# Kernel tuning notes

Measured on AMD Instinct MI355X. Metric: run time of the kernel, lower is better.

Reference implementation:

```python
import jax, jax.numpy as jnp
import numpy as np

IMG_H, IMG_W = 1024, 1024
STRIDES = (8, 16, 32, 64, 128)
NUM_CLASSES = 80
CONF_THR = 0.05
IOU_THR = 0.5
MAX_PER_CLASS = 100
MAX_DET = 100
K_CAND = 256  # candidates kept per class before greedy NMS (pre-sort cap)


def build_grids():
    gy, gx, gs = [], [], []
    for s in STRIDES:
        H, W = IMG_H // s, IMG_W // s
        h = jnp.arange(H, dtype=jnp.float32)
        w = jnp.arange(W, dtype=jnp.float32)
        gy_, gx_ = jnp.meshgrid(h, w)  # 'xy' indexing -> shape [W, H], matches tf.meshgrid
        gy.append(gy_.reshape(-1))
        gx.append(gx_.reshape(-1))
        gs.append(jnp.full((W * H,), float(s), dtype=jnp.float32))
    return jnp.concatenate(gy), jnp.concatenate(gx), jnp.concatenate(gs)


def pairwise_iou(b):
    # b: [K,4] as (y1, x1, y2, x2)
    y1, x1, y2, x2 = b[:, 0], b[:, 1], b[:, 2], b[:, 3]
    area = (y2 - y1) * (x2 - x1)
    ih = jnp.maximum(jnp.minimum(y2[:, None], y2[None, :]) - jnp.maximum(y1[:, None], y1[None, :]), 0.0)
    iw = jnp.maximum(jnp.minimum(x2[:, None], x2[None, :]) - jnp.maximum(x1[:, None], x1[None, :]), 0.0)
    inter = ih * iw
    union = area[:, None] + area[None, :] - inter
    return inter / jnp.maximum(union, 1e-8)


def nms_one_class(boxes, scores):
    # boxes [N,4], scores [N] -> (sel_boxes [MAX_PER_CLASS,4], sel_scores [MAX_PER_CLASS])
    top_s, idx = jax.lax.top_k(scores, K_CAND)
    cand = boxes[idx]                       # [K,4]
    valid = top_s > CONF_THR
    iou = jax.lax.stop_gradient(pairwise_iou(cand))  # suppression mask is non-differentiable
    rng = jnp.arange(K_CAND)

    def body(i, keep):
        sup = (iou[i] > IOU_THR) & (rng > i) & keep[i]
        return keep & ~sup

    keep = jax.lax.fori_loop(0, K_CAND, body, valid)
    kept = jnp.where(keep, top_s, 0.0)
    sel_s, sel_i = jax.lax.top_k(kept, MAX_PER_CLASS)
    return cand[sel_i], sel_s


def combined_nms(boxes, scores):
    # per image: boxes [N,4] shared across classes, scores [N,C]
    cls_boxes, cls_scores = jax.vmap(nms_one_class, in_axes=(None, 1))(boxes, scores)
    C = scores.shape[1]
    cls_labels = jnp.broadcast_to(jnp.arange(C, dtype=jnp.float32)[:, None], cls_scores.shape)
    flat_s = cls_scores.reshape(-1)
    flat_b = cls_boxes.reshape(-1, 4)
    flat_l = cls_labels.reshape(-1)
    fin_s, fin_i = jax.lax.top_k(flat_s, MAX_DET)
    fin_b = flat_b[fin_i] * (fin_s > 0.0)[:, None].astype(flat_b.dtype)  # zero pad boxes like TF
    fin_l = flat_l[fin_i]
    return fin_b, fin_l, fin_s


def decode(pred_regs, pred_ctrs, pred_clfs):
    gy, gx, gs = build_grids()
    gy, gx, gs = gy[:, None], gx[:, None], gs[:, None]     # [N,1]
    score = pred_clfs * pred_ctrs                           # [B,N,C]
    x1 = gx - pred_regs[..., 0:1]
    x2 = gx + pred_regs[..., 1:2]
    y1 = gy - pred_regs[..., 2:3]
    y2 = gy + pred_regs[..., 3:4]
    bbox = jnp.concatenate([y1, x1, y2, x2], axis=-1) * gs  # [B,N,4] in image coords
    return jax.vmap(combined_nms)(bbox, score)


def setup_inputs() -> dict:
    key = jax.random.key(0)
    k1, k2, k3 = jax.random.split(key, 3)
    N = sum((IMG_H // s) * (IMG_W // s) for s in STRIDES)  # 21824
    B = 16
    return {
        "pred_regs": jax.random.uniform(k1, (B, N, 4), jnp.float32),
        "pred_ctrs": jax.random.uniform(k2, (B, N, 1), jnp.float32),
        "pred_clfs": jax.random.uniform(k3, (B, N, NUM_CLASSES), jnp.float32),
    }


def reference(pred_regs, pred_ctrs, pred_clfs):
    # returns (final_bboxes [B,100,4], final_labels [B,100] float, final_scores [B,100])
    return decode(pred_regs, pred_ctrs, pred_clfs)
```

## Files before the change

### kernel.cpp

```cpp
#include <hip/hip_runtime.h>
#include <stdint.h>

#pragma clang fp contract(off)

namespace {
constexpr int kN = 21824;
constexpr int kB = 16;
constexpr int kC = 80;
constexpr int kK = 256;
constexpr int kMaxPC = 100;
constexpr int kMaxDet = 100;
constexpr int kBins1 = 2048;
constexpr int kCap = 1536;
constexpr int kSortN = 512;
constexpr int kRows = kB * kC;
constexpr int kTiles = kN / 64;
constexpr int kTPB = 6;
constexpr int kGScan = (kTiles + kTPB - 1) / kTPB;
constexpr int kLCap = 48;
constexpr float kThr = 0.72f;
constexpr int kTasks = 1152;
}

__device__ __forceinline__ uint64_t make_key(float s, int n) {
  return ((uint64_t)__float_as_uint(s) << 16) | (uint32_t)(0xFFFF - n);
}

__device__ uint32_t block_scan_incl(uint32_t val) {
  __shared__ uint32_t wsum[4];
  int lane = threadIdx.x & 63;
  int wave = threadIdx.x >> 6;
  for (int d = 1; d < 64; d <<= 1) {
    uint32_t t = __shfl_up(val, (unsigned)d, 64);
    if (lane >= d) val += t;
  }
  if (lane == 63) wsum[wave] = val;
  __syncthreads();
  uint32_t off = 0;
  for (int w = 0; w < wave; ++w) off += wsum[w];
  __syncthreads();
  return val + off;
}

struct RegSrc {
  uint64_t k[6];
  int cnt;
  template <class F> __device__ void each(F f) const {
    #pragma unroll
    for (int j = 0; j < 6; ++j)
      if (j < cnt) f(k[j]);
  }
  template <class F> __device__ void each2(F f) const {
    #pragma unroll
    for (int j = 0; j < 6; ++j) f(k[j], j < cnt);
  }
};
struct ColSrc {
  const float* cl;
  const float* ct;
  template <class F> __device__ void each(F f) const {
    for (int n = threadIdx.x; n < kN; n += 256)
      f(make_key(cl[(size_t)n * kC] * ct[n], n));
  }
  template <class F> __device__ void each2(F f) const {
    constexpr int kNr = (kN + 255) & ~255;
    for (int n = threadIdx.x; n < kNr; n += 256) {
      bool v = n < kN;
      float s = v ? cl[(size_t)n * kC] * ct[n] : 0.0f;
      f(make_key(s, n), v);
    }
  }
};
struct ArrSrc {
  const float* s;
  int count;
  template <class F> __device__ void each(F f) const {
    for (int i = threadIdx.x; i < count; i += 256) f(make_key(s[i], i));
  }
  template <class F> __device__ void each2(F f) const {
    int cr = (count + 255) & ~255;
    for (int i = threadIdx.x; i < cr; i += 256) {
      bool v = i < count;
      float sv = v ? s[i] : 0.0f;
      f(make_key(sv, i), v);
    }
  }
};

template <class Src, bool FAST>
__device__ int refine_gather(const Src& src, int K, int cap,
                             uint32_t* hist, uint64_t* cbuf) {
  __shared__ int sel_bin;
  __shared__ uint32_t sel_hd, sel_above, qcnt;
  int tid = threadIdx.x;

  for (int i = tid; i < kBins1; i += 256) hist[i] = 0;
  __syncthreads();
  src.each([&](uint64_t k) {
    uint32_t bin = FAST ? (uint32_t)((k >> 28) & 0x7FF) : (uint32_t)(k >> 37);
    atomicAdd(&hist[bin], 1u);
  });
  __syncthreads();
  uint32_t krem = (uint32_t)K;
  {
    uint32_t bl[8], v = 0;
    int base = kBins1 - 1 - 8 * tid;
    for (int j = 0; j < 8; ++j) { bl[j] = hist[base - j]; v += bl[j]; }
    uint32_t S = block_scan_incl(v);
    if (S >= krem && (S - v) < krem) {
      uint32_t cum = S - v;
      for (int j = 0; j < 8; ++j) {
        cum += bl[j];
        if (cum >= krem) { sel_bin = base - j; sel_hd = bl[j]; sel_above = cum - bl[j]; break; }
      }
    }
    __syncthreads();
  }
  uint64_t prefix = FAST ? (uint64_t)(0x3F000u | (uint32_t)sel_bin)
                         : (uint64_t)sel_bin;
  int shift = FAST ? 28 : 37;
  krem = (uint32_t)K - sel_above;
  uint32_t Sge = ((uint32_t)K - krem) + sel_hd;
  __syncthreads();

  while (Sge > (uint32_t)cap) {
    int w = (shift > 8) ? 8 : shift;
    int ns = shift - w, bins = 1 << w, hs = shift;
    for (int i = tid; i < bins; i += 256) hist[i] = 0;
    __syncthreads();
    uint64_t pfx = prefix;
    src.each([&](uint64_t k) {
      if ((k >> hs) == pfx)
        atomicAdd(&hist[(uint32_t)(k >> ns) & (bins - 1)], 1u);
    });
    __syncthreads();
    uint32_t v = (tid < bins) ? hist[bins - 1 - tid] : 0;
    uint32_t S = block_scan_incl(v);
    if (v && S >= krem && (S - v) < krem) {
      sel_bin = bins - 1 - tid; sel_hd = v; sel_above = S - v;
    }
    __syncthreads();
    prefix = (prefix << w) | (uint32_t)sel_bin;
    krem -= sel_above;
    Sge = ((uint32_t)K - krem) + sel_hd;
    shift = ns;
    __syncthreads();
  }

  uint64_t L = prefix << shift;
  if (tid == 0) qcnt = 0;
  __syncthreads();
  {
    int lane = tid & 63;
    uint64_t lmask = (1ull << lane) - 1ull;
    src.each2([&](uint64_t k, bool valid) {
      bool q = valid && (k >= L);
      unsigned long long m = __ballot(q);
      uint32_t base = 0;
      if (lane == 0 && m) base = atomicAdd(&qcnt, (uint32_t)__popcll(m));
      base = __shfl(base, 0, 64);
      if (q) {
        uint32_t p = base + (uint32_t)__popcll(m & lmask);
        if (p < (uint32_t)cap) cbuf[p] = k;
      }
    });
  }
  __syncthreads();
  int Scnt = (int)qcnt;
  return Scnt > cap ? cap : Scnt;
}

__device__ __forceinline__ void bitonic512_desc(uint64_t* sortb) {
  int tid = threadIdx.x;
  uint64_t e0 = sortb[2 * tid], e1 = sortb[2 * tid + 1];
  #pragma unroll
  for (int k2 = 2; k2 <= kSortN; k2 <<= 1) {
    #pragma unroll
    for (int j = k2 >> 1; j >= 2; j >>= 1) {
      bool up = ((tid & (k2 >> 1)) == 0);
      uint64_t p0, p1;
      bool low;
      if (j >= 128) {
        __syncthreads();
        sortb[2 * tid] = e0; sortb[2 * tid + 1] = e1;
        __syncthreads();
        int pi = (2 * tid) ^ j;
        p0 = sortb[pi]; p1 = sortb[pi + 1];
        low = ((tid & (j >> 1)) == 0);
      } else {
        int d = j >> 1;
        p0 = (uint64_t)__shfl_xor((unsigned long long)e0, d, 64);
        p1 = (uint64_t)__shfl_xor((unsigned long long)e1, d, 64);
        low = ((tid & d) == 0);
      }
      bool keepMax = (up == low);
      e0 = (keepMax == (e0 > p0)) ? e0 : p0;
      e1 = (keepMax == (e1 > p1)) ? e1 : p1;
    }
    {
      bool up = ((tid & (k2 >> 1)) == 0);
      bool sw = up ? (e0 < e1) : (e0 > e1);
      uint64_t t0 = sw ? e1 : e0, t1 = sw ? e0 : e1;
      e0 = t0; e1 = t1;
    }
  }
  __syncthreads();
  sortb[2 * tid] = e0; sortb[2 * tid + 1] = e1;
  __syncthreads();
}

__global__ __launch_bounds__(256) void score_scan_kernel(
    const float* __restrict__ clfs, const float* __restrict__ ctrs,
    uint32_t* __restrict__ gcnt, uint64_t* __restrict__ glist) {
  int b = blockIdx.y;
  int t0 = blockIdx.x * kTPB;
  int t1 = t0 + kTPB; if (t1 > kTiles) t1 = kTiles;
  int nbase = t0 * 64;
  int nanch = (t1 - t0) * 64;

  __shared__ uint64_t lbuf[kC][kLCap + 1];
  __shared__ uint32_t lcnt[kC];
  __shared__ uint32_t gbase[kC];
  __shared__ float ct[kTPB * 64];
  int tid = threadIdx.x;
  for (int i = tid; i < kC; i += 256) lcnt[i] = 0;
  for (int i = tid; i < nanch; i += 256) ct[i] = ctrs[(size_t)b * kN + nbase + i];
  __syncthreads();

  const float4* src = (const float4*)(clfs + ((size_t)b * kN + nbase) * kC);
  int n4 = nanch * (kC / 4);
  float4 v = (tid < n4) ? src[tid] : float4{0, 0, 0, 0};
  for (int e = tid; e < n4; e += 256) {
    int en = e + 256;
    float4 vn = (en < n4) ? src[en] : float4{0, 0, 0, 0};
    int a = e / 20;
    int c0 = (e % 20) * 4;
    float cv = ct[a];
    int n = nbase + a;
    float sv[4] = {v.x * cv, v.y * cv, v.z * cv, v.w * cv};
    #pragma unroll
    for (int j = 0; j < 4; ++j) {
      if (sv[j] > kThr) {
        int c = c0 + j;
        uint32_t p = atomicAdd(&lcnt[c], 1u);
        if (p < kLCap) lbuf[c][p] = make_key(sv[j], n);
      }
    }
    v = vn;
  }
  __syncthreads();

  if (tid < kC) {
    uint32_t m = lcnt[tid];
    int row = b * kC + tid;
    if (m > kLCap) {
      atomicAdd(&gcnt[row], (uint32_t)(kCap + 1));
      gbase[tid] = 0xFFFFFFFFu;
    } else {
      gbase[tid] = m ? atomicAdd(&gcnt[row], m) : 0u;
    }
  }
  __syncthreads();

  int lane = tid & 63, wave = tid >> 6;
  for (int c = wave * 20; c < wave * 20 + 20; ++c) {
    uint32_t m = lcnt[c];
    uint32_t base = gbase[c];
    if (base == 0xFFFFFFFFu || m == 0) continue;
    if (m > kLCap) m = kLCap;
    int row = b * kC + c;
    for (uint32_t i = lane; i < m; i += 64) {
      uint32_t p = base + i;
      if (p < kCap) glist[(size_t)row * kCap + p] = lbuf[c][i];
    }
  }
}

__global__ __launch_bounds__(256) void nms_class_kernel(
    const uint32_t* __restrict__ gcnt, const uint64_t* __restrict__ glist,
    const float* __restrict__ clfs, const float* __restrict__ ctrs,
    const float* __restrict__ regs,
    float* __restrict__ cls_boxes, float* __restrict__ cls_scores) {
  int row = blockIdx.x;
  int b = row / kC, c = row % kC;
  int tid = threadIdx.x;
  int lane = tid & 63, wave = tid >> 6;

  __shared__ union alignas(16) {
    uint32_t hist[kBins1];
    uint64_t sortb[kSortN];
    uint32_t supm[kK][8];
  } hu;
  __shared__ float4 boxf4[kK];
  __shared__ float barea[kK];
  __shared__ uint32_t rnz[8];
  __shared__ uint64_t kinit[4];
  __shared__ uint64_t kfin[4];

  uint32_t cnt = gcnt[row];
  int Scnt;
  if (cnt >= (uint32_t)kK && cnt <= (uint32_t)kCap) {
    RegSrc rs; rs.cnt = 0;
    const uint64_t* gl = glist + (size_t)row * kCap;
    #pragma unroll
    for (int j = 0; j < 6; ++j) {
      int i = tid + j * 256;
      if (i < (int)cnt) { rs.k[j] = gl[i]; rs.cnt = j + 1; }
    }
    Scnt = refine_gather<RegSrc, true>(rs, kK, kSortN, hu.hist, hu.sortb);
  } else {
    ColSrc cs{clfs + (size_t)b * kN * kC + c, ctrs + (size_t)b * kN};
    Scnt = refine_gather<ColSrc, false>(cs, kK, kSortN, hu.hist, hu.sortb);
  }

  for (int i = Scnt + tid; i < kSortN; i += 256) hu.sortb[i] = 0;
  __syncthreads();
  bitonic512_desc(hu.sortb);
  uint64_t myk = hu.sortb[tid];
  __syncthreads();

  int n = 0xFFFF - (int)(myk & 0xFFFF);
  float sc_v = __uint_as_float((uint32_t)(myk >> 16));
  int off, hl;
  float sf;
  if (n < 16384)      { off = 0;     hl = 7; sf = 8.f;   }
  else if (n < 20480) { off = 16384; hl = 6; sf = 16.f;  }
  else if (n < 21504) { off = 20480; hl = 5; sf = 32.f;  }
  else if (n < 21760) { off = 21504; hl = 4; sf = 64.f;  }
  else                { off = 21760; hl = 3; sf = 128.f; }
  int kk = n - off;
  float gx = (float)(kk >> hl);
  float gy = (float)(kk & ((1 << hl) - 1));
  const float4 r = ((const float4*)regs)[(size_t)b * kN + n];
  float4 mybox;
  mybox.x = (gy - r.z) * sf;
  mybox.y = (gx - r.x) * sf;
  mybox.z = (gy + r.w) * sf;
  mybox.w = (gx + r.y) * sf;
  float my_a = (mybox.z - mybox.x) * (mybox.w - mybox.y);
  boxf4[tid] = mybox;
  barea[tid] = my_a;
  unsigned long long vm = __ballot(sc_v > 0.05f);
  if (lane == 0) kinit[wave] = vm;
  {
    uint64_t* sp = (uint64_t*)&hu.supm[0][0];
    #pragma unroll
    for (int q = 0; q < 4; ++q) sp[tid + q * 256] = 0;
    if (tid < 8) rnz[tid] = 0;
  }
  __syncthreads();

  for (int t = tid; t < kTasks; t += 256) {
    int w = (t >= 32) + (t >= 96) + (t >= 192) + (t >= 320) +
            (t >= 480) + (t >= 672) + (t >= 896);
    int rr = t - 16 * w * (w + 1);
    float4 A = boxf4[rr];
    float aA = barea[rr];
    const float4* bp = boxf4 + (w << 5);
    const float* ap = barea + (w << 5);
    uint32_t cur = 0;
    #pragma unroll
    for (int s = 0; s < 32; ++s) {
      const float4 Bx = bp[s];
      float aB = ap[s];
      float yy1 = fmaxf(A.x, Bx.x);
      float yy2 = fminf(A.z, Bx.z);
      float xx1 = fmaxf(A.y, Bx.y);
      float xx2 = fminf(A.w, Bx.w);
      float ih = fmaxf(yy2 - yy1, 0.0f);
      float iw = fmaxf(xx2 - xx1, 0.0f);
      float inter = ih * iw;
      float un = (aB + aA) - inter;
      float unc = fmaxf(un, 1e-8f);
      cur |= (inter + inter > unc) ? (1u << s) : 0u;
    }
    uint32_t mask = (w == (rr >> 5)) ? (0xFFFFFFFEu << (rr & 31)) : 0xFFFFFFFFu;
    cur &= mask;
    hu.supm[rr][w] = cur;
    if (cur) atomicOr(&rnz[rr >> 5], 1u << (rr & 31));
  }
  __syncthreads();

  if (wave == 0) {
    uint64_t kw0 = kinit[0], kw1 = kinit[1], kw2 = kinit[2], kw3 = kinit[3];
    uint64_t wn0 = rnz[0] | ((uint64_t)rnz[1] << 32);
    uint64_t wn1 = rnz[2] | ((uint64_t)rnz[3] << 32);
    uint64_t wn2 = rnz[4] | ((uint64_t)rnz[5] << 32);
    uint64_t wn3 = rnz[6] | ((uint64_t)rnz[7] << 32);
    #define NMS_SECTION(W, KW, WN)                                          \
      _Pragma("unroll")                                                     \
      for (int ch = 0; ch < 16; ++ch) {                                     \
        if ((WN >> (ch * 4)) & 0xFull) {                                    \
          const ulonglong2* s0 = (const ulonglong2*)hu.supm[(W << 6) + ch * 4 + 0]; \
          const ulonglong2* s1 = (const ulonglong2*)hu.supm[(W << 6) + ch * 4 + 1]; \
          const ulonglong2* s2 = (const ulonglong2*)hu.supm[(W << 6) + ch * 4 + 2]; \
          const ulonglong2* s3 = (const ulonglong2*)hu.supm[(W << 6) + ch * 4 + 3]; \
          ulonglong2 aL = s0[0], aH = s0[1];                                \
          ulonglong2 bL = s1[0], bH = s1[1];                                \
          ulonglong2 cL = s2[0], cH = s2[1];                                \
          ulonglong2 dL = s3[0], dH = s3[1];                                \
          if ((KW >> (ch * 4 + 0)) & 1ull) { kw0 &= ~aL.x; kw1 &= ~aL.y; kw2 &= ~aH.x; kw3 &= ~aH.y; } \
          if ((KW >> (ch * 4 + 1)) & 1ull) { kw0 &= ~bL.x; kw1 &= ~bL.y; kw2 &= ~bH.x; kw3 &= ~bH.y; } \
          if ((KW >> (ch * 4 + 2)) & 1ull) { kw0 &= ~cL.x; kw1 &= ~cL.y; kw2 &= ~cH.x; kw3 &= ~cH.y; } \
          if ((KW >> (ch * 4 + 3)) & 1ull) { kw0 &= ~dL.x; kw1 &= ~dL.y; kw2 &= ~dH.x; kw3 &= ~dH.y; } \
        }                                                                   \
      }
    NMS_SECTION(0, kw0, wn0)
    NMS_SECTION(1, kw1, wn1)
    NMS_SECTION(2, kw2, wn2)
    NMS_SECTION(3, kw3, wn3)
    #undef NMS_SECTION
    if (lane == 0) { kfin[0] = kw0; kfin[1] = kw1; kfin[2] = kw2; kfin[3] = kw3; }
  }
  __syncthreads();

  uint64_t kw0 = kfin[0], kw1 = kfin[1], kw2 = kfin[2], kw3 = kfin[3];
  uint64_t ww = (wave == 0) ? kw0 : (wave == 1) ? kw1 : (wave == 2) ? kw2 : kw3;
  bool keptf = (ww >> lane) & 1ull;
  int kept_total = (int)(__popcll(kw0) + __popcll(kw1) +
                         __popcll(kw2) + __popcll(kw3));
  int kept_before = (int)__popcll(ww & ((1ull << lane) - 1ull));
  if (wave > 0) kept_before += (int)__popcll(kw0);
  if (wave > 1) kept_before += (int)__popcll(kw1);
  if (wave > 2) kept_before += (int)__popcll(kw2);

  int rank2 = keptf ? kept_before : (kept_total + tid - kept_before);
  if (rank2 < kMaxPC) {
    float ks = keptf ? sc_v : 0.0f;
    size_t obase = ((size_t)row) * kMaxPC + rank2;
    cls_scores[obase] = ks;
    float* ob = cls_boxes + obase * 4;
    ob[0] = mybox.x; ob[1] = mybox.y; ob[2] = mybox.z; ob[3] = mybox.w;
  }
}

__global__ __launch_bounds__(256) void final_topk_kernel(
    const float* __restrict__ cls_scores, const float* __restrict__ cls_boxes,
    float* __restrict__ out) {
  int b = blockIdx.x;
  int tid = threadIdx.x;
  const int M = kC * kMaxPC;
  __shared__ union alignas(16) {
    uint32_t hist[kBins1];
    uint64_t sortb[kSortN];
  } hu;

  ArrSrc as{cls_scores + (size_t)b * M, M};
  int Scnt = refine_gather<ArrSrc, false>(as, kMaxDet, kSortN, hu.hist, hu.sortb);

  for (int i = Scnt + tid; i < kSortN; i += 256) hu.sortb[i] = 0;
  __syncthreads();
  bitonic512_desc(hu.sortb);

  if (tid < kMaxDet) {
    uint64_t myk = hu.sortb[tid];
    float sv = __uint_as_float((uint32_t)(myk >> 16));
    int f = 0xFFFF - (int)(myk & 0xFFFF);
    int cls = f / 100;
    const float* bp = cls_boxes + ((size_t)b * M + f) * 4;
    float m = (sv > 0.0f) ? 1.0f : 0.0f;
    float* ob = out + ((size_t)b * kMaxDet + tid) * 4;
    ob[0] = bp[0] * m; ob[1] = bp[1] * m; ob[2] = bp[2] * m; ob[3] = bp[3] * m;
    out[(size_t)kB * kMaxDet * 4 + (size_t)b * kMaxDet + tid] = (float)cls;
    out[(size_t)kB * kMaxDet * 5 + (size_t)b * kMaxDet + tid] = sv;
  }
}

extern "C" void kernel_launch(void* const* d_in, const int* in_sizes, int n_in,
                              void* d_out, int out_size, void* d_ws, size_t ws_size,
                              hipStream_t stream) {
  (void)in_sizes; (void)n_in; (void)out_size;
  const float* regs = (const float*)d_in[0];
  const float* ctrs = (const float*)d_in[1];
  const float* clfs = (const float*)d_in[2];
  float* out = (float*)d_out;

  const size_t glB  = (size_t)kRows * kCap * sizeof(uint64_t);
  const size_t cbB  = (size_t)kRows * kMaxPC * 4 * sizeof(float);
  const size_t csB  = (size_t)kRows * kMaxPC * sizeof(float);
  const size_t cntB = 8192;
  if (ws_size < glB + cbB + csB + cntB) return;

  char* p = (char*)d_ws;
  uint64_t* glist   = (uint64_t*)p; p += glB;
  float* cls_boxes  = (float*)p;    p += cbB;
  float* cls_scores = (float*)p;    p += csB;
  uint32_t* gcnt    = (uint32_t*)p;

  hipMemsetAsync(gcnt, 0, (size_t)kRows * sizeof(uint32_t), stream);
  score_scan_kernel<<<dim3(kGScan, kB), 256, 0, stream>>>(clfs, ctrs, gcnt, glist);
  nms_class_kernel<<<kRows, 256, 0, stream>>>(gcnt, glist, clfs, ctrs, regs,
                                              cls_boxes, cls_scores);
  final_topk_kernel<<<kB, 256, 0, stream>>>(cls_scores, cls_boxes, out);
}
```

Before: 242.9 us.

## Fuse final top-k into NMS kernel via last-block counter and prefetch box regs

Removes the separate final_topk launch: each class block increments a per-image counter after a threadfence, and the last block for that image runs the final top-k inline. The candidate keys now carry their gather slot index, so box regressions can be loaded and decoded before the bitonic sort and looked up by slot afterwards, overlapping global latency with the sort. The score scan also replaces the per-element divide and modulo with incremental index tracking. In exchange the tail work becomes serialized in one block per image, and there is an extra shared buffer and barrier.

Result: slower. 352.1 us (+45.0%).

```diff
diff --git a/kernel.cpp b/kernel.cpp
--- a/kernel.cpp
+++ b/kernel.cpp
@@ -161,7 +161,7 @@
       base = __shfl(base, 0, 64);
       if (q) {
         uint32_t p = base + (uint32_t)__popcll(m & lmask);
-        if (p < (uint32_t)cap) cbuf[p] = k;
+        if (p < (uint32_t)cap) cbuf[p] = (k << 16) | p;
       }
     });
   }
@@ -209,6 +209,25 @@
   __syncthreads();
 }
 
+__device__ __forceinline__ float4 decode_box(const float4& r, int n) {
+  int off, hl;
+  float sf;
+  if (n < 16384)      { off = 0;     hl = 7; sf = 8.f;   }
+  else if (n < 20480) { off = 16384; hl = 6; sf = 16.f;  }
+  else if (n < 21504) { off = 20480; hl = 5; sf = 32.f;  }
+  else if (n < 21760) { off = 21504; hl = 4; sf = 64.f;  }
+  else                { off = 21760; hl = 3; sf = 128.f; }
+  int kk = n - off;
+  float gx = (float)(kk >> hl);
+  float gy = (float)(kk & ((1 << hl) - 1));
+  float4 bx;
+  bx.x = (gy - r.z) * sf;
+  bx.y = (gx - r.x) * sf;
+  bx.z = (gy + r.w) * sf;
+  bx.w = (gx + r.y) * sf;
+  return bx;
+}
+
 __global__ __launch_bounds__(256) void score_scan_kernel(
     const float* __restrict__ clfs, const float* __restrict__ ctrs,
     uint32_t* __restrict__ gcnt, uint64_t* __restrict__ glist) {
@@ -230,11 +249,12 @@
   const float4* src = (const float4*)(clfs + ((size_t)b * kN + nbase) * kC);
   int n4 = nanch * (kC / 4);
   float4 v = (tid < n4) ? src[tid] : float4{0, 0, 0, 0};
+  int a = tid / 20;
+  int rem = tid - a * 20;
   for (int e = tid; e < n4; e += 256) {
     int en = e + 256;
     float4 vn = (en < n4) ? src[en] : float4{0, 0, 0, 0};
-    int a = e / 20;
-    int c0 = (e % 20) * 4;
+    int c0 = rem * 4;
     float cv = ct[a];
     int n = nbase + a;
     float sv[4] = {v.x * cv, v.y * cv, v.z * cv, v.w * cv};
@@ -247,6 +267,8 @@
       }
     }
     v = vn;
+    a += 12; rem += 16;
+    if (rem >= 20) { rem -= 20; ++a; }
   }
   __syncthreads();
 
@@ -276,11 +298,36 @@
   }
 }
 
+__device__ void final_topk_block(int b, const float* cls_scores,
+                                 const float* cls_boxes, float* out,
+                                 uint32_t* hist, uint64_t* sbuf) {
+  int tid = threadIdx.x;
+  const int M = kC * kMaxPC;
+  ArrSrc as{cls_scores + (size_t)b * M, M};
+  int Scnt = refine_gather<ArrSrc, false>(as, kMaxDet, kSortN, hist, sbuf);
+  for (int i = Scnt + tid; i < kSortN; i += 256) sbuf[i] = 0;
+  __syncthreads();
+  bitonic512_desc(sbuf);
+  if (tid < kMaxDet) {
+    uint64_t myk = sbuf[tid] >> 16;
+    float sv = __uint_as_float((uint32_t)(myk >> 16));
+    int f = 0xFFFF - (int)(myk & 0xFFFF);
+    int cls = f / 100;
+    const float* bp = cls_boxes + ((size_t)b * M + f) * 4;
+    float m = (sv > 0.0f) ? 1.0f : 0.0f;
+    float* ob = out + ((size_t)b * kMaxDet + tid) * 4;
+    ob[0] = bp[0] * m; ob[1] = bp[1] * m; ob[2] = bp[2] * m; ob[3] = bp[3] * m;
+    out[(size_t)kB * kMaxDet * 4 + (size_t)b * kMaxDet + tid] = (float)cls;
+    out[(size_t)kB * kMaxDet * 5 + (size_t)b * kMaxDet + tid] = sv;
+  }
+}
+
 __global__ __launch_bounds__(256) void nms_class_kernel(
-    const uint32_t* __restrict__ gcnt, const uint64_t* __restrict__ glist,
+    uint32_t* gcnt, const uint64_t* __restrict__ glist,
     const float* __restrict__ clfs, const float* __restrict__ ctrs,
     const float* __restrict__ regs,
-    float* __restrict__ cls_boxes, float* __restrict__ cls_scores) {
+    float* __restrict__ cls_boxes, float* __restrict__ cls_scores,
+    float* __restrict__ out) {
   int row = blockIdx.x;
   int b = row / kC, c = row % kC;
   int tid = threadIdx.x;
@@ -288,14 +335,16 @@
 
   __shared__ union alignas(16) {
     uint32_t hist[kBins1];
-    uint64_t sortb[kSortN];
     uint32_t supm[kK][8];
+    float4 boxq[kSortN];
   } hu;
+  __shared__ uint64_t sbuf[kSortN];
   __shared__ float4 boxf4[kK];
   __shared__ float barea[kK];
   __shared__ uint32_t rnz[8];
   __shared__ uint64_t kinit[4];
   __shared__ uint64_t kfin[4];
+  __shared__ uint32_t bflag;
 
   uint32_t cnt = gcnt[row];
   int Scnt;
@@ -307,41 +356,42 @@
       int i = tid + j * 256;
       if (i < (int)cnt) { rs.k[j] = gl[i]; rs.cnt = j + 1; }
     }
-    Scnt = refine_gather<RegSrc, true>(rs, kK, kSortN, hu.hist, hu.sortb);
+    Scnt = refine_gather<RegSrc, true>(rs, kK, kSortN, hu.hist, sbuf);
   } else {
     ColSrc cs{clfs + (size_t)b * kN * kC + c, ctrs + (size_t)b * kN};
-    Scnt = refine_gather<ColSrc, false>(cs, kK, kSortN, hu.hist, hu.sortb);
-  }
-
-  for (int i = Scnt + tid; i < kSortN; i += 256) hu.sortb[i] = 0;
-  __syncthreads();
-  bitonic512_desc(hu.sortb);
-  uint64_t myk = hu.sortb[tid];
-  __syncthreads();
-
-  int n = 0xFFFF - (int)(myk & 0xFFFF);
+    Scnt = refine_gather<ColSrc, false>(cs, kK, kSortN, hu.hist, sbuf);
+  }
+
+  for (int i = Scnt + tid; i < kSortN; i += 256) sbuf[i] = 0;
+  __syncthreads();
+
+  uint64_t E0 = sbuf[2 * tid], E1 = sbuf[2 * tid + 1];
+  int p0 = (int)(E0 & 0xFFFF), p1 = (int)(E1 & 0xFFFF);
+  int a0 = 0xFFFF - (int)((E0 >> 16) & 0xFFFF);
+  int a1 = 0xFFFF - (int)((E1 >> 16) & 0xFFFF);
+  int a0v = (E0 != 0) ? a0 : 0;
+  int a1v = (E1 != 0) ? a1 : 0;
+  const float4* rp = (const float4*)regs + (size_t)b * kN;
+  float4 r0 = rp[a0v];
+  float4 r1 = rp[a1v];
+
+  bitonic512_desc(sbuf);
+
+  if (E0 != 0) hu.boxq[p0] = decode_box(r0, a0v);
+  if (E1 != 0) hu.boxq[p1] = decode_box(r1, a1v);
+  __syncthreads();
+
+  uint64_t ku = sbuf[tid];
+  uint32_t qidx = (uint32_t)(ku & 0xFFFF);
+  uint64_t myk = ku >> 16;
   float sc_v = __uint_as_float((uint32_t)(myk >> 16));
-  int off, hl;
-  float sf;
-  if (n < 16384)      { off = 0;     hl = 7; sf = 8.f;   }
-  else if (n < 20480) { off = 16384; hl = 6; sf = 16.f;  }
-  else if (n < 21504) { off = 20480; hl = 5; sf = 32.f;  }
-  else if (n < 21760) { off = 21504; hl = 4; sf = 64.f;  }
-  else                { off = 21760; hl = 3; sf = 128.f; }
-  int kk = n - off;
-  float gx = (float)(kk >> hl);
-  float gy = (float)(kk & ((1 << hl) - 1));
-  const float4 r = ((const float4*)regs)[(size_t)b * kN + n];
-  float4 mybox;
-  mybox.x = (gy - r.z) * sf;
-  mybox.y = (gx - r.x) * sf;
-  mybox.z = (gy + r.w) * sf;
-  mybox.w = (gx + r.y) * sf;
+  float4 mybox = hu.boxq[qidx];
   float my_a = (mybox.z - mybox.x) * (mybox.w - mybox.y);
   boxf4[tid] = mybox;
   barea[tid] = my_a;
   unsigned long long vm = __ballot(sc_v > 0.05f);
   if (lane == 0) kinit[wave] = vm;
+  __syncthreads();
   {
     uint64_t* sp = (uint64_t*)&hu.supm[0][0];
     #pragma unroll
@@ -432,37 +482,17 @@
     float* ob = cls_boxes + obase * 4;
     ob[0] = mybox.x; ob[1] = mybox.y; ob[2] = mybox.z; ob[3] = mybox.w;
   }
-}
-
-__global__ __launch_bounds__(256) void final_topk_kernel(
-    const float* __restrict__ cls_scores, const float* __restrict__ cls_boxes,
-    float* __restrict__ out) {
-  int b = blockIdx.x;
-  int tid = threadIdx.x;
-  const int M = kC * kMaxPC;
-  __shared__ union alignas(16) {
-    uint32_t hist[kBins1];
-    uint64_t sortb[kSortN];
-  } hu;
-
-  ArrSrc as{cls_scores + (size_t)b * M, M};
-  int Scnt = refine_gather<ArrSrc, false>(as, kMaxDet, kSortN, hu.hist, hu.sortb);
-
-  for (int i = Scnt + tid; i < kSortN; i += 256) hu.sortb[i] = 0;
-  __syncthreads();
-  bitonic512_desc(hu.sortb);
-
-  if (tid < kMaxDet) {
-    uint64_t myk = hu.sortb[tid];
-    float sv = __uint_as_float((uint32_t)(myk >> 16));
-    int f = 0xFFFF - (int)(myk & 0xFFFF);
-    int cls = f / 100;
-    const float* bp = cls_boxes + ((size_t)b * M + f) * 4;
-    float m = (sv > 0.0f) ? 1.0f : 0.0f;
-    float* ob = out + ((size_t)b * kMaxDet + tid) * 4;
-    ob[0] = bp[0] * m; ob[1] = bp[1] * m; ob[2] = bp[2] * m; ob[3] = bp[3] * m;
-    out[(size_t)kB * kMaxDet * 4 + (size_t)b * kMaxDet + tid] = (float)cls;
-    out[(size_t)kB * kMaxDet * 5 + (size_t)b * kMaxDet + tid] = sv;
+
+  __threadfence();
+  __syncthreads();
+  if (tid == 0) {
+    uint32_t old = atomicAdd(&gcnt[kRows + b], 1u);
+    bflag = (old == (uint32_t)(kC - 1)) ? 1u : 0u;
+  }
+  __syncthreads();
+  if (bflag) {
+    __threadfence();
+    final_topk_block(b, cls_scores, cls_boxes, out, hu.hist, sbuf);
   }
 }
 
@@ -487,9 +517,8 @@
   float* cls_scores = (float*)p;    p += csB;
   uint32_t* gcnt    = (uint32_t*)p;
 
-  hipMemsetAsync(gcnt, 0, (size_t)kRows * sizeof(uint32_t), stream);
+  hipMemsetAsync(gcnt, 0, (size_t)(kRows + kB) * sizeof(uint32_t), stream);
   score_scan_kernel<<<dim3(kGScan, kB), 256, 0, stream>>>(clfs, ctrs, gcnt, glist);
   nms_class_kernel<<<kRows, 256, 0, stream>>>(gcnt, glist, clfs, ctrs, regs,
-                                              cls_boxes, cls_scores);
-  final_topk_kernel<<<kB, 256, 0, stream>>>(cls_scores, cls_boxes, out);
-}
+                                              cls_boxes, cls_scores, out);
+}
```
